# Kernel optimization log

Hardware: AMD Instinct MI355X
Metric: run time of the kernel (lower is better)

The kernel has to match this reference:

```python
import jax, jax.numpy as jnp
import numpy as np

N_BASIS = 8
N_RANK = 4
IN_DIM = 64
B, T = 64, 8192


def _make_projections():
    # Match torch module: np.random.seed(15385); per rank draw E then F, QR, take first n_basis cols.
    np.random.seed(seed=15385)
    Es, Fs = [], []
    for _ in range(N_RANK):
        G = np.random.standard_normal([IN_DIM, IN_DIM])
        Q, _ = np.linalg.qr(G)
        Es.append(Q[:, :N_BASIS])
        G = np.random.standard_normal([IN_DIM, IN_DIM])
        Q, _ = np.linalg.qr(G)
        Fs.append(Q[:, :N_BASIS])
    E = jnp.asarray(np.stack(Es), dtype=jnp.float32)  # [R, C, nb]
    F = jnp.asarray(np.stack(Fs), dtype=jnp.float32)  # [R, C, nb]
    return E, F


def setup_inputs() -> dict:
    key = jax.random.key(0)
    x = jax.random.normal(key, (B, IN_DIM, T), dtype=jnp.float32)
    E, F = _make_projections()
    init_sigma = float(np.sqrt(IN_DIM))
    sigma = jnp.full((N_RANK,), init_sigma, dtype=jnp.float32)
    rho = jnp.full((N_RANK,), init_sigma, dtype=jnp.float32)
    return {"x": x, "sigma": sigma, "rho": rho, "E": E, "F": F}


def reference(x, sigma, rho, E, F):
    # x: [B, C, T]; E,F: [R, C, nb]; sigma,rho: [R]
    in_dim = x.shape[1]
    scale = jnp.sqrt(jnp.float32(in_dim))
    Er = (scale / (1e-05 + jnp.abs(sigma)))[:, None, None] * E  # [R, C, nb]
    Fr = (scale / (1e-05 + jnp.abs(rho)))[:, None, None] * F    # [R, C, nb]
    xe = jnp.einsum('bct,rcn->brtn', x, Er)  # [B, R, T, nb]
    xf = jnp.einsum('bct,rcm->brtm', x, Fr)  # [B, R, T, nb]
    # outer product per (b, t), summed over rank, averaged
    z = jnp.einsum('brtn,brtm->btnm', xe, xf) / jnp.float32(N_RANK)  # [B, T, nb, nb]
    bsz, tlen = x.shape[0], x.shape[2]
    out = z.reshape(bsz, tlen, N_BASIS * N_BASIS).transpose(0, 2, 1)  # [B, nb^2, T]
    # use_normalization=True: signed sqrt + channel max normalization
    out = jnp.sign(out) * (jnp.sqrt(jnp.abs(out) + 0.01) - jnp.float32(np.sqrt(0.01)))
    max_vals = jnp.max(jnp.abs(out), axis=1, keepdims=True)
    out = out / (max_vals + 1e-05)
    return out
```

## Files before the change

### kernel.cpp

```cpp
#include <hip/hip_runtime.h>

#define BB 64
#define CC 64
#define TT 8192
#define NB 8

typedef __attribute__((ext_vector_type(8))) short bf16x8;
typedef __attribute__((ext_vector_type(4))) float f32x4;
typedef __attribute__((ext_vector_type(4))) int i32x4;

union I4B8 { i32x4 i; bf16x8 b; };

__device__ __forceinline__ unsigned short f32_to_bf16_rn(float f) {
    unsigned u = __float_as_uint(f);
    unsigned r = (u + 0x7FFFu + ((u >> 16) & 1u)) >> 16;
    return (unsigned short)r;
}
__device__ __forceinline__ float bf16_to_f32(unsigned short h) {
    return __uint_as_float(((unsigned)h) << 16);
}

__global__ __launch_bounds__(256) void rpg_prep(
    const float* __restrict__ sigma, const float* __restrict__ rho,
    const float* __restrict__ E, const float* __restrict__ F,
    unsigned short* __restrict__ Wf)
{
    const int idx = blockIdx.x * 256 + threadIdx.x;
    if (idx >= 8192) return;
    const int j    = idx & 7;
    const int slot = idx >> 3;
    const int lane = slot & 63;
    const int h    = (slot >> 6) & 1;
    const int ks   = (slot >> 7) & 1;
    const int mt   = (slot >> 8) & 3;
    const int p = mt * 16 + (lane & 15);
    const int c = ks * 32 + (lane >> 4) * 8 + j;
    float val;
    if (p < 32) {
        const int r = p >> 3, n = p & 7;
        const float es = 8.0f / (1e-5f + fabsf(sigma[r]));
        const float fs = 8.0f / (1e-5f + fabsf(rho[r]));
        val = E[r * (CC * NB) + c * NB + n] * (es * fs * 0.25f);
    } else {
        const int r = (p - 32) >> 3, n = p & 7;
        val = F[r * (CC * NB) + c * NB + n];
    }
    const unsigned short hi = f32_to_bf16_rn(val);
    Wf[idx] = (h == 0) ? hi : f32_to_bf16_rn(val - bf16_to_f32(hi));
}

__global__ __launch_bounds__(256, 8) void rpg_main(
    const float* __restrict__ x,
    const unsigned short* __restrict__ Wf,
    float* __restrict__ out)
{
    __shared__ __align__(16) char smem[16384];
    char* xhs = smem;
    char* xls = smem + 8192;

    const int tid  = threadIdx.x;
    const int w    = tid >> 6;
    const int lane = tid & 63;
    const int am   = lane & 15;
    const int ag   = lane >> 4;

    const int b  = blockIdx.x >> 7;
    const int t0 = (blockIdx.x & 127) * 64;

    {
        const float* xcol = x + b * (CC * TT) + t0 + lane;
        unsigned hw[8], lw[8];
        #pragma unroll
        for (int k = 0; k < 8; ++k) {
            const int c = w * 16 + 2 * k;
            const float f0 = xcol[(c    ) * TT];
            const float f1 = xcol[(c + 1) * TT];
            const unsigned u0 = __float_as_uint(f0), u1 = __float_as_uint(f1);
            hw[k] = (u0 >> 16) | (u1 & 0xFFFF0000u);
            const float h0 = __uint_as_float(u0 & 0xFFFF0000u);
            const float h1 = __uint_as_float(u1 & 0xFFFF0000u);
            lw[k] = (__float_as_uint(f0 - h0) >> 16) | (__float_as_uint(f1 - h1) & 0xFFFF0000u);
        }
        const int sw = lane & 7;
        char* hb = xhs + lane * 128;
        char* lb = xls + lane * 128;
        *(i32x4*)(hb + (((2 * w    ) ^ sw) * 16)) = (i32x4){(int)hw[0], (int)hw[1], (int)hw[2], (int)hw[3]};
        *(i32x4*)(hb + (((2 * w + 1) ^ sw) * 16)) = (i32x4){(int)hw[4], (int)hw[5], (int)hw[6], (int)hw[7]};
        *(i32x4*)(lb + (((2 * w    ) ^ sw) * 16)) = (i32x4){(int)lw[0], (int)lw[1], (int)lw[2], (int)lw[3]};
        *(i32x4*)(lb + (((2 * w + 1) ^ sw) * 16)) = (i32x4){(int)lw[4], (int)lw[5], (int)lw[6], (int)lw[7]};
    }
    __syncthreads();

    bf16x8 xh[2], xl[2];
    {
        const int trow = w * 16 + am;
        const int sw   = trow & 7;
        #pragma unroll
        for (int ks = 0; ks < 2; ++ks) {
            const int g  = (ks * 4 + ag) ^ sw;
            const int off = trow * 128 + g * 16;
            xh[ks] = ((const I4B8*)(xhs + off))->b;
            xl[ks] = ((const I4B8*)(xls + off))->b;
        }
    }

    f32x4 acc[4];
    #pragma unroll
    for (int mt = 0; mt < 4; ++mt) {
        acc[mt] = (f32x4){0.0f, 0.0f, 0.0f, 0.0f};
        #pragma unroll
        for (int ks = 0; ks < 2; ++ks) {
            const bf16x8 wh = *(const bf16x8*)(Wf + (((mt * 2 + ks) * 2 + 0) * 64 + lane) * 8);
            const bf16x8 wl = *(const bf16x8*)(Wf + (((mt * 2 + ks) * 2 + 1) * 64 + lane) * 8);
            acc[mt] = __builtin_amdgcn_mfma_f32_16x16x32_bf16(wh, xh[ks], acc[mt], 0, 0, 0);
            acc[mt] = __builtin_amdgcn_mfma_f32_16x16x32_bf16(wh, xl[ks], acc[mt], 0, 0, 0);
            acc[mt] = __builtin_amdgcn_mfma_f32_16x16x32_bf16(wl, xh[ks], acc[mt], 0, 0, 0);
        }
    }

    const bool ra0 = (ag & 2) == 0;
    const bool qlo = (ag & 1) == 0;

    float pA[4], pB[4], pC[4], pD[4];
    #pragma unroll
    for (int i = 0; i < 4; ++i) {
        pA[i] = __shfl_xor(acc[0][i], 32);
        pB[i] = __shfl_xor(acc[1][i], 32);
        pC[i] = __shfl_xor(acc[2][i], 32);
        pD[i] = __shfl_xor(acc[3][i], 32);
    }

    float xe_[4][2];
    #pragma unroll
    for (int e = 0; e < 2; ++e) {
        xe_[0][e] = ra0 ? acc[0][e] : pA[2 + e];
        xe_[1][e] = ra0 ? pA[e]     : acc[0][2 + e];
        xe_[2][e] = ra0 ? acc[1][e] : pB[2 + e];
        xe_[3][e] = ra0 ? pB[e]     : acc[1][2 + e];
    }

    float xfq0[4], xfq1[4], xfq2[4], xfq3[4];
    #pragma unroll
    for (int i = 0; i < 4; ++i) {
        xfq0[i] = ra0 ? acc[2][i] : pC[i];
        xfq1[i] = ra0 ? pC[i]     : acc[2][i];
        xfq2[i] = ra0 ? acc[3][i] : pD[i];
        xfq3[i] = ra0 ? pD[i]     : acc[3][i];
    }
    float xfo0[4], xfo1[4], xfo2[4], xfo3[4];
    #pragma unroll
    for (int i = 0; i < 4; ++i) {
        xfo0[i] = __shfl_xor(xfq0[i], 16);
        xfo1[i] = __shfl_xor(xfq1[i], 16);
        xfo2[i] = __shfl_xor(xfq2[i], 16);
        xfo3[i] = __shfl_xor(xfq3[i], 16);
    }
    float xfL[4][4], xfH[4][4];
    #pragma unroll
    for (int i = 0; i < 4; ++i) {
        xfL[0][i] = qlo ? xfq0[i] : xfo0[i];  xfH[0][i] = qlo ? xfo0[i] : xfq0[i];
        xfL[1][i] = qlo ? xfq1[i] : xfo1[i];  xfH[1][i] = qlo ? xfo1[i] : xfq1[i];
        xfL[2][i] = qlo ? xfq2[i] : xfo2[i];  xfH[2][i] = qlo ? xfo2[i] : xfq2[i];
        xfL[3][i] = qlo ? xfq3[i] : xfo3[i];  xfH[3][i] = qlo ? xfo3[i] : xfq3[i];
    }

    float z[2][8];
    float pm = 0.0f;
    #pragma unroll
    for (int e = 0; e < 2; ++e) {
        #pragma unroll
        for (int m = 0; m < 4; ++m) {
            float a = xe_[0][e] * xfL[0][m];
            a = fmaf(xe_[1][e], xfL[1][m], a);
            a = fmaf(xe_[2][e], xfL[2][m], a);
            a = fmaf(xe_[3][e], xfL[3][m], a);
            float s = __builtin_amdgcn_sqrtf(fabsf(a) + 0.01f) - 0.1f;
            float v = copysignf(s, a);
            z[e][m] = v;
            pm = fmaxf(pm, fabsf(v));
        }
        #pragma unroll
        for (int m = 0; m < 4; ++m) {
            float a = xe_[0][e] * xfH[0][m];
            a = fmaf(xe_[1][e], xfH[1][m], a);
            a = fmaf(xe_[2][e], xfH[2][m], a);
            a = fmaf(xe_[3][e], xfH[3][m], a);
            float s = __builtin_amdgcn_sqrtf(fabsf(a) + 0.01f) - 0.1f;
            float v = copysignf(s, a);
            z[e][4 + m] = v;
            pm = fmaxf(pm, fabsf(v));
        }
    }

    pm = fmaxf(pm, __shfl_xor(pm, 16));
    pm = fmaxf(pm, __shfl_xor(pm, 32));
    const float rinv = __builtin_amdgcn_rcpf(pm + 1e-5f);

    const int nbase = (qlo ? 0 : 4) + (ra0 ? 0 : 2);
    float* ob = out + b * (64 * TT) + t0 + w * 16 + am;
    #pragma unroll
    for (int e = 0; e < 2; ++e)
        #pragma unroll
        for (int m = 0; m < 8; ++m)
            ob[((nbase + e) * NB + m) * TT] = z[e][m] * rinv;
}

extern "C" void kernel_launch(void* const* d_in, const int* in_sizes, int n_in,
                              void* d_out, int out_size, void* d_ws, size_t ws_size,
                              hipStream_t stream) {
    const float* x     = (const float*)d_in[0];
    const float* sigma = (const float*)d_in[1];
    const float* rho   = (const float*)d_in[2];
    const float* E     = (const float*)d_in[3];
    const float* F     = (const float*)d_in[4];
    float* out = (float*)d_out;

    unsigned short* Wf = (unsigned short*)d_ws;

    rpg_prep<<<32, 256, 0, stream>>>(sigma, rho, E, F, Wf);

    dim3 grid(BB * (TT / 64));
    dim3 block(256);
    rpg_main<<<grid, block, 0, stream>>>(x, Wf, out);
}
```

Baseline: 60.67 us.

## Fuse weight prep into persistent kernel with double-buffered x prefetch

Removes the separate weight-preparation kernel: each block now builds the bf16 hi/lo split weights in shared memory itself. The main kernel becomes persistent with a fixed grid of 768 blocks looping over 8192 windows. It prefetches the next window's x into registers while computing the current one, using double-buffered LDS. This saves a launch and global weight loads, at the cost of lower occupancy (48KB LDS, launch bounds 3) and redundant per-block weight setup.

New measurement: 49.84 us. 17.9% less time.

```diff
diff --git a/kernel.cpp b/kernel.cpp
--- a/kernel.cpp
+++ b/kernel.cpp
@@ -1,9 +1,10 @@
 #include <hip/hip_runtime.h>
 
-#define BB 64
 #define CC 64
 #define TT 8192
 #define NB 8
+#define NWIN 8192
+#define GRID 768
 
 typedef __attribute__((ext_vector_type(8))) short bf16x8;
 typedef __attribute__((ext_vector_type(4))) float f32x4;
@@ -20,43 +21,16 @@
     return __uint_as_float(((unsigned)h) << 16);
 }
 
-__global__ __launch_bounds__(256) void rpg_prep(
-    const float* __restrict__ sigma, const float* __restrict__ rho,
-    const float* __restrict__ E, const float* __restrict__ F,
-    unsigned short* __restrict__ Wf)
-{
-    const int idx = blockIdx.x * 256 + threadIdx.x;
-    if (idx >= 8192) return;
-    const int j    = idx & 7;
-    const int slot = idx >> 3;
-    const int lane = slot & 63;
-    const int h    = (slot >> 6) & 1;
-    const int ks   = (slot >> 7) & 1;
-    const int mt   = (slot >> 8) & 3;
-    const int p = mt * 16 + (lane & 15);
-    const int c = ks * 32 + (lane >> 4) * 8 + j;
-    float val;
-    if (p < 32) {
-        const int r = p >> 3, n = p & 7;
-        const float es = 8.0f / (1e-5f + fabsf(sigma[r]));
-        const float fs = 8.0f / (1e-5f + fabsf(rho[r]));
-        val = E[r * (CC * NB) + c * NB + n] * (es * fs * 0.25f);
-    } else {
-        const int r = (p - 32) >> 3, n = p & 7;
-        val = F[r * (CC * NB) + c * NB + n];
-    }
-    const unsigned short hi = f32_to_bf16_rn(val);
-    Wf[idx] = (h == 0) ? hi : f32_to_bf16_rn(val - bf16_to_f32(hi));
-}
-
-__global__ __launch_bounds__(256, 8) void rpg_main(
+__global__ __launch_bounds__(256, 3) void rpg_fused(
     const float* __restrict__ x,
-    const unsigned short* __restrict__ Wf,
+    const float* __restrict__ sigma,
+    const float* __restrict__ rho,
+    const float* __restrict__ E,
+    const float* __restrict__ F,
     float* __restrict__ out)
 {
-    __shared__ __align__(16) char smem[16384];
-    char* xhs = smem;
-    char* xls = smem + 8192;
+    __shared__ __align__(16) char smem[49152];
+    char* wsl = smem;
 
     const int tid  = threadIdx.x;
     const int w    = tid >> 6;
@@ -64,145 +38,207 @@
     const int am   = lane & 15;
     const int ag   = lane >> 4;
 
-    const int b  = blockIdx.x >> 7;
-    const int t0 = (blockIdx.x & 127) * 64;
-
     {
+        const int r = tid >> 6;
+        const int c = tid & 63;
+        const float g = (8.0f / (1e-5f + fabsf(sigma[r]))) *
+                        (8.0f / (1e-5f + fabsf(rho[r]))) * 0.25f;
+        const int wks = c >> 5, wag = (c >> 3) & 3, wj = c & 7;
+        const float4 e0 = *(const float4*)(E + (r * 64 + c) * 8);
+        const float4 e1 = *(const float4*)(E + (r * 64 + c) * 8 + 4);
+        const float4 fv0 = *(const float4*)(F + (r * 64 + c) * 8);
+        const float4 fv1 = *(const float4*)(F + (r * 64 + c) * 8 + 4);
+        const float ev[8] = {e0.x, e0.y, e0.z, e0.w, e1.x, e1.y, e1.z, e1.w};
+        const float fv[8] = {fv0.x, fv0.y, fv0.z, fv0.w, fv1.x, fv1.y, fv1.z, fv1.w};
+        #pragma unroll
+        for (int n = 0; n < 8; ++n) {
+            {
+                const int p = r * 8 + n;
+                const float val = ev[n] * g;
+                const unsigned short hi = f32_to_bf16_rn(val);
+                const unsigned short lo = f32_to_bf16_rn(val - bf16_to_f32(hi));
+                const int mt = p >> 4, pam = p & 15;
+                char* base = wsl + ((((mt * 2 + wks) * 2 + 0) * 64 + wag * 16 + pam) << 4) + wj * 2;
+                *(unsigned short*)base = hi;
+                *(unsigned short*)(base + 1024) = lo;
+            }
+            {
+                const int p = 32 + r * 8 + n;
+                const float val = fv[n];
+                const unsigned short hi = f32_to_bf16_rn(val);
+                const unsigned short lo = f32_to_bf16_rn(val - bf16_to_f32(hi));
+                const int mt = p >> 4, pam = p & 15;
+                char* base = wsl + ((((mt * 2 + wks) * 2 + 0) * 64 + wag * 16 + pam) << 4) + wj * 2;
+                *(unsigned short*)base = hi;
+                *(unsigned short*)(base + 1024) = lo;
+            }
+        }
+    }
+
+    int wid = blockIdx.x;
+    float f[16];
+    {
+        const int b = wid >> 7, t0 = (wid & 127) << 6;
         const float* xcol = x + b * (CC * TT) + t0 + lane;
-        unsigned hw[8], lw[8];
-        #pragma unroll
-        for (int k = 0; k < 8; ++k) {
-            const int c = w * 16 + 2 * k;
-            const float f0 = xcol[(c    ) * TT];
-            const float f1 = xcol[(c + 1) * TT];
-            const unsigned u0 = __float_as_uint(f0), u1 = __float_as_uint(f1);
-            hw[k] = (u0 >> 16) | (u1 & 0xFFFF0000u);
-            const float h0 = __uint_as_float(u0 & 0xFFFF0000u);
-            const float h1 = __uint_as_float(u1 & 0xFFFF0000u);
-            lw[k] = (__float_as_uint(f0 - h0) >> 16) | (__float_as_uint(f1 - h1) & 0xFFFF0000u);
-        }
-        const int sw = lane & 7;
-        char* hb = xhs + lane * 128;
-        char* lb = xls + lane * 128;
-        *(i32x4*)(hb + (((2 * w    ) ^ sw) * 16)) = (i32x4){(int)hw[0], (int)hw[1], (int)hw[2], (int)hw[3]};
-        *(i32x4*)(hb + (((2 * w + 1) ^ sw) * 16)) = (i32x4){(int)hw[4], (int)hw[5], (int)hw[6], (int)hw[7]};
-        *(i32x4*)(lb + (((2 * w    ) ^ sw) * 16)) = (i32x4){(int)lw[0], (int)lw[1], (int)lw[2], (int)lw[3]};
-        *(i32x4*)(lb + (((2 * w + 1) ^ sw) * 16)) = (i32x4){(int)lw[4], (int)lw[5], (int)lw[6], (int)lw[7]};
+        #pragma unroll
+        for (int k = 0; k < 16; ++k) f[k] = xcol[(w * 16 + k) * TT];
     }
-    __syncthreads();
-
-    bf16x8 xh[2], xl[2];
-    {
-        const int trow = w * 16 + am;
-        const int sw   = trow & 7;
-        #pragma unroll
-        for (int ks = 0; ks < 2; ++ks) {
-            const int g  = (ks * 4 + ag) ^ sw;
-            const int off = trow * 128 + g * 16;
-            xh[ks] = ((const I4B8*)(xhs + off))->b;
-            xl[ks] = ((const I4B8*)(xls + off))->b;
-        }
-    }
-
-    f32x4 acc[4];
-    #pragma unroll
-    for (int mt = 0; mt < 4; ++mt) {
-        acc[mt] = (f32x4){0.0f, 0.0f, 0.0f, 0.0f};
-        #pragma unroll
-        for (int ks = 0; ks < 2; ++ks) {
-            const bf16x8 wh = *(const bf16x8*)(Wf + (((mt * 2 + ks) * 2 + 0) * 64 + lane) * 8);
-            const bf16x8 wl = *(const bf16x8*)(Wf + (((mt * 2 + ks) * 2 + 1) * 64 + lane) * 8);
-            acc[mt] = __builtin_amdgcn_mfma_f32_16x16x32_bf16(wh, xh[ks], acc[mt], 0, 0, 0);
-            acc[mt] = __builtin_amdgcn_mfma_f32_16x16x32_bf16(wh, xl[ks], acc[mt], 0, 0, 0);
-            acc[mt] = __builtin_amdgcn_mfma_f32_16x16x32_bf16(wl, xh[ks], acc[mt], 0, 0, 0);
-        }
-    }
-
+
+    int ibuf = 0;
     const bool ra0 = (ag & 2) == 0;
     const bool qlo = (ag & 1) == 0;
 
-    float pA[4], pB[4], pC[4], pD[4];
-    #pragma unroll
-    for (int i = 0; i < 4; ++i) {
-        pA[i] = __shfl_xor(acc[0][i], 32);
-        pB[i] = __shfl_xor(acc[1][i], 32);
-        pC[i] = __shfl_xor(acc[2][i], 32);
-        pD[i] = __shfl_xor(acc[3][i], 32);
+    while (wid < NWIN) {
+        char* xbuf = ibuf ? (smem + 32768) : (smem + 16384);
+
+        {
+            unsigned hw[8], lw[8];
+            #pragma unroll
+            for (int k = 0; k < 8; ++k) {
+                const unsigned u0 = __float_as_uint(f[2 * k]);
+                const unsigned u1 = __float_as_uint(f[2 * k + 1]);
+                hw[k] = (u0 >> 16) | (u1 & 0xFFFF0000u);
+                const float h0 = __uint_as_float(u0 & 0xFFFF0000u);
+                const float h1 = __uint_as_float(u1 & 0xFFFF0000u);
+                lw[k] = (__float_as_uint(f[2 * k] - h0) >> 16) |
+                        (__float_as_uint(f[2 * k + 1] - h1) & 0xFFFF0000u);
+            }
+            const int sw = lane & 7;
+            char* hb = xbuf + lane * 128;
+            char* lb = xbuf + 8192 + lane * 128;
+            *(i32x4*)(hb + (((2 * w    ) ^ sw) * 16)) = (i32x4){(int)hw[0], (int)hw[1], (int)hw[2], (int)hw[3]};
+            *(i32x4*)(hb + (((2 * w + 1) ^ sw) * 16)) = (i32x4){(int)hw[4], (int)hw[5], (int)hw[6], (int)hw[7]};
+            *(i32x4*)(lb + (((2 * w    ) ^ sw) * 16)) = (i32x4){(int)lw[0], (int)lw[1], (int)lw[2], (int)lw[3]};
+            *(i32x4*)(lb + (((2 * w + 1) ^ sw) * 16)) = (i32x4){(int)lw[4], (int)lw[5], (int)lw[6], (int)lw[7]};
+        }
+
+        const int b  = wid >> 7;
+        const int t0 = (wid & 127) << 6;
+        const int next = wid + GRID;
+
+        __syncthreads();
+
+        bf16x8 xh[2], xl[2];
+        {
+            const int trow = w * 16 + am;
+            const int sw   = trow & 7;
+            #pragma unroll
+            for (int ks = 0; ks < 2; ++ks) {
+                const int g2  = (ks * 4 + ag) ^ sw;
+                const int off = trow * 128 + g2 * 16;
+                xh[ks] = ((const I4B8*)(xbuf + off))->b;
+                xl[ks] = ((const I4B8*)(xbuf + 8192 + off))->b;
+            }
+        }
+
+        if (next < NWIN) {
+            const int nbx = next >> 7, nt0 = (next & 127) << 6;
+            const float* xcol = x + nbx * (CC * TT) + nt0 + lane;
+            #pragma unroll
+            for (int k = 0; k < 16; ++k) f[k] = xcol[(w * 16 + k) * TT];
+        }
+
+        f32x4 acc[4];
+        #pragma unroll
+        for (int mt = 0; mt < 4; ++mt) {
+            acc[mt] = (f32x4){0.0f, 0.0f, 0.0f, 0.0f};
+            #pragma unroll
+            for (int ks = 0; ks < 2; ++ks) {
+                const int fb = ((mt * 2 + ks) * 2) * 1024 + lane * 16;
+                const bf16x8 wh = ((const I4B8*)(wsl + fb))->b;
+                const bf16x8 wl = ((const I4B8*)(wsl + fb + 1024))->b;
+                acc[mt] = __builtin_amdgcn_mfma_f32_16x16x32_bf16(wh, xh[ks], acc[mt], 0, 0, 0);
+                acc[mt] = __builtin_amdgcn_mfma_f32_16x16x32_bf16(wh, xl[ks], acc[mt], 0, 0, 0);
+                acc[mt] = __builtin_amdgcn_mfma_f32_16x16x32_bf16(wl, xh[ks], acc[mt], 0, 0, 0);
+            }
+        }
+
+        float pA[4], pB[4], pC[4], pD[4];
+        #pragma unroll
+        for (int i = 0; i < 4; ++i) {
+            pA[i] = __shfl_xor(acc[0][i], 32);
+            pB[i] = __shfl_xor(acc[1][i], 32);
+            pC[i] = __shfl_xor(acc[2][i], 32);
+            pD[i] = __shfl_xor(acc[3][i], 32);
+        }
+
+        float xe_[4][2];
+        #pragma unroll
+        for (int e = 0; e < 2; ++e) {
+            xe_[0][e] = ra0 ? acc[0][e] : pA[2 + e];
+            xe_[1][e] = ra0 ? pA[e]     : acc[0][2 + e];
+            xe_[2][e] = ra0 ? acc[1][e] : pB[2 + e];
+            xe_[3][e] = ra0 ? pB[e]     : acc[1][2 + e];
+        }
+
+        float xfq0[4], xfq1[4], xfq2[4], xfq3[4];
+        #pragma unroll
+        for (int i = 0; i < 4; ++i) {
+            xfq0[i] = ra0 ? acc[2][i] : pC[i];
+            xfq1[i] = ra0 ? pC[i]     : acc[2][i];
+            xfq2[i] = ra0 ? acc[3][i] : pD[i];
+            xfq3[i] = ra0 ? pD[i]     : acc[3][i];
+        }
+        float xfo0[4], xfo1[4], xfo2[4], xfo3[4];
+        #pragma unroll
+        for (int i = 0; i < 4; ++i) {
+            xfo0[i] = __shfl_xor(xfq0[i], 16);
+            xfo1[i] = __shfl_xor(xfq1[i], 16);
+            xfo2[i] = __shfl_xor(xfq2[i], 16);
+            xfo3[i] = __shfl_xor(xfq3[i], 16);
+        }
+        float xfL[4][4], xfH[4][4];
+        #pragma unroll
+        for (int i = 0; i < 4; ++i) {
+            xfL[0][i] = qlo ? xfq0[i] : xfo0[i];  xfH[0][i] = qlo ? xfo0[i] : xfq0[i];
+            xfL[1][i] = qlo ? xfq1[i] : xfo1[i];  xfH[1][i] = qlo ? xfo1[i] : xfq1[i];
+            xfL[2][i] = qlo ? xfq2[i] : xfo2[i];  xfH[2][i] = qlo ? xfo2[i] : xfq2[i];
+            xfL[3][i] = qlo ? xfq3[i] : xfo3[i];  xfH[3][i] = qlo ? xfo3[i] : xfq3[i];
+        }
+
+        float z[2][8];
+        float pm = 0.0f;
+        #pragma unroll
+        for (int e = 0; e < 2; ++e) {
+            #pragma unroll
+            for (int m = 0; m < 4; ++m) {
+                float a = xe_[0][e] * xfL[0][m];
+                a = fmaf(xe_[1][e], xfL[1][m], a);
+                a = fmaf(xe_[2][e], xfL[2][m], a);
+                a = fmaf(xe_[3][e], xfL[3][m], a);
+                float s = __builtin_amdgcn_sqrtf(fabsf(a) + 0.01f) - 0.1f;
+                float v = copysignf(s, a);
+                z[e][m] = v;
+                pm = fmaxf(pm, fabsf(v));
+            }
+            #pragma unroll
+            for (int m = 0; m < 4; ++m) {
+                float a = xe_[0][e] * xfH[0][m];
+                a = fmaf(xe_[1][e], xfH[1][m], a);
+                a = fmaf(xe_[2][e], xfH[2][m], a);
+                a = fmaf(xe_[3][e], xfH[3][m], a);
+                float s = __builtin_amdgcn_sqrtf(fabsf(a) + 0.01f) - 0.1f;
+                float v = copysignf(s, a);
+                z[e][4 + m] = v;
+                pm = fmaxf(pm, fabsf(v));
+            }
+        }
+
+        pm = fmaxf(pm, __shfl_xor(pm, 16));
+        pm = fmaxf(pm, __shfl_xor(pm, 32));
+        const float rinv = __builtin_amdgcn_rcpf(pm + 1e-5f);
+
+        const int nbase = (qlo ? 0 : 4) + (ra0 ? 0 : 2);
+        float* ob = out + b * (64 * TT) + t0 + w * 16 + am;
+        #pragma unroll
+        for (int e = 0; e < 2; ++e)
+            #pragma unroll
+            for (int m = 0; m < 8; ++m)
+                ob[((nbase + e) * NB + m) * TT] = z[e][m] * rinv;
+
+        wid = next;
+        ibuf ^= 1;
     }
-
-    float xe_[4][2];
-    #pragma unroll
-    for (int e = 0; e < 2; ++e) {
-        xe_[0][e] = ra0 ? acc[0][e] : pA[2 + e];
-        xe_[1][e] = ra0 ? pA[e]     : acc[0][2 + e];
-        xe_[2][e] = ra0 ? acc[1][e] : pB[2 + e];
-        xe_[3][e] = ra0 ? pB[e]     : acc[1][2 + e];
-    }
-
-    float xfq0[4], xfq1[4], xfq2[4], xfq3[4];
-    #pragma unroll
-    for (int i = 0; i < 4; ++i) {
-        xfq0[i] = ra0 ? acc[2][i] : pC[i];
-        xfq1[i] = ra0 ? pC[i]     : acc[2][i];
-        xfq2[i] = ra0 ? acc[3][i] : pD[i];
-        xfq3[i] = ra0 ? pD[i]     : acc[3][i];
-    }
-    float xfo0[4], xfo1[4], xfo2[4], xfo3[4];
-    #pragma unroll
-    for (int i = 0; i < 4; ++i) {
-        xfo0[i] = __shfl_xor(xfq0[i], 16);
-        xfo1[i] = __shfl_xor(xfq1[i], 16);
-        xfo2[i] = __shfl_xor(xfq2[i], 16);
-        xfo3[i] = __shfl_xor(xfq3[i], 16);
-    }
-    float xfL[4][4], xfH[4][4];
-    #pragma unroll
-    for (int i = 0; i < 4; ++i) {
-        xfL[0][i] = qlo ? xfq0[i] : xfo0[i];  xfH[0][i] = qlo ? xfo0[i] : xfq0[i];
-        xfL[1][i] = qlo ? xfq1[i] : xfo1[i];  xfH[1][i] = qlo ? xfo1[i] : xfq1[i];
-        xfL[2][i] = qlo ? xfq2[i] : xfo2[i];  xfH[2][i] = qlo ? xfo2[i] : xfq2[i];
-        xfL[3][i] = qlo ? xfq3[i] : xfo3[i];  xfH[3][i] = qlo ? xfo3[i] : xfq3[i];
-    }
-
-    float z[2][8];
-    float pm = 0.0f;
-    #pragma unroll
-    for (int e = 0; e < 2; ++e) {
-        #pragma unroll
-        for (int m = 0; m < 4; ++m) {
-            float a = xe_[0][e] * xfL[0][m];
-            a = fmaf(xe_[1][e], xfL[1][m], a);
-            a = fmaf(xe_[2][e], xfL[2][m], a);
-            a = fmaf(xe_[3][e], xfL[3][m], a);
-            float s = __builtin_amdgcn_sqrtf(fabsf(a) + 0.01f) - 0.1f;
-            float v = copysignf(s, a);
-            z[e][m] = v;
-            pm = fmaxf(pm, fabsf(v));
-        }
-        #pragma unroll
-        for (int m = 0; m < 4; ++m) {
-            float a = xe_[0][e] * xfH[0][m];
-            a = fmaf(xe_[1][e], xfH[1][m], a);
-            a = fmaf(xe_[2][e], xfH[2][m], a);
-            a = fmaf(xe_[3][e], xfH[3][m], a);
-            float s = __builtin_amdgcn_sqrtf(fabsf(a) + 0.01f) - 0.1f;
-            float v = copysignf(s, a);
-            z[e][4 + m] = v;
-            pm = fmaxf(pm, fabsf(v));
-        }
-    }
-
-    pm = fmaxf(pm, __shfl_xor(pm, 16));
-    pm = fmaxf(pm, __shfl_xor(pm, 32));
-    const float rinv = __builtin_amdgcn_rcpf(pm + 1e-5f);
-
-    const int nbase = (qlo ? 0 : 4) + (ra0 ? 0 : 2);
-    float* ob = out + b * (64 * TT) + t0 + w * 16 + am;
-    #pragma unroll
-    for (int e = 0; e < 2; ++e)
-        #pragma unroll
-        for (int m = 0; m < 8; ++m)
-            ob[((nbase + e) * NB + m) * TT] = z[e][m] * rinv;
 }
 
 extern "C" void kernel_launch(void* const* d_in, const int* in_sizes, int n_in,
@@ -215,11 +251,5 @@
     const float* F     = (const float*)d_in[4];
     float* out = (float*)d_out;
 
-    unsigned short* Wf = (unsigned short*)d_ws;
-
-    rpg_prep<<<32, 256, 0, stream>>>(sigma, rho, E, F, Wf);
-
-    dim3 grid(BB * (TT / 64));
-    dim3 block(256);
-    rpg_main<<<grid, block, 0, stream>>>(x, Wf, out);
-}
+    rpg_fused<<<GRID, 256, 0, stream>>>(x, sigma, rho, E, F, out);
+}
```

## Use persistent waves with register-prefetched x tiles and no LDS staging

Applied to the files above, without the earlier changes.

Replaces the one-block-per-64-timesteps grid with a persistent grid of 768 blocks. Each wave loops over 16-timestep tiles and prefetches the next tile's x into registers while it computes the current one. The split weights are loaded into registers once per wave instead of per tile. Each lane now loads x directly in MFMA operand layout, which removes the LDS staging buffer and the barrier. Global loads become 16-wide in t rather than 64-wide, which may reduce coalescing, and register pressure rises.

Result: faster. 59.28 us (-2.3%).

```diff
diff --git a/kernel.cpp b/kernel.cpp
--- a/kernel.cpp
+++ b/kernel.cpp
@@ -1,9 +1,11 @@
 #include <hip/hip_runtime.h>
 
-#define BB 64
 #define CC 64
 #define TT 8192
 #define NB 8
+#define NW16 32768
+#define GRID 768
+#define NWAVES (GRID * 4)
 
 typedef __attribute__((ext_vector_type(8))) short bf16x8;
 typedef __attribute__((ext_vector_type(4))) float f32x4;
@@ -49,160 +51,177 @@
     Wf[idx] = (h == 0) ? hi : f32_to_bf16_rn(val - bf16_to_f32(hi));
 }
 
-__global__ __launch_bounds__(256, 8) void rpg_main(
+__global__ __launch_bounds__(256, 3) void rpg_main(
     const float* __restrict__ x,
     const unsigned short* __restrict__ Wf,
     float* __restrict__ out)
 {
-    __shared__ __align__(16) char smem[16384];
-    char* xhs = smem;
-    char* xls = smem + 8192;
-
     const int tid  = threadIdx.x;
     const int w    = tid >> 6;
     const int lane = tid & 63;
     const int am   = lane & 15;
     const int ag   = lane >> 4;
 
-    const int b  = blockIdx.x >> 7;
-    const int t0 = (blockIdx.x & 127) * 64;
-
-    {
-        const float* xcol = x + b * (CC * TT) + t0 + lane;
-        unsigned hw[8], lw[8];
-        #pragma unroll
-        for (int k = 0; k < 8; ++k) {
-            const int c = w * 16 + 2 * k;
-            const float f0 = xcol[(c    ) * TT];
-            const float f1 = xcol[(c + 1) * TT];
-            const unsigned u0 = __float_as_uint(f0), u1 = __float_as_uint(f1);
-            hw[k] = (u0 >> 16) | (u1 & 0xFFFF0000u);
-            const float h0 = __uint_as_float(u0 & 0xFFFF0000u);
-            const float h1 = __uint_as_float(u1 & 0xFFFF0000u);
-            lw[k] = (__float_as_uint(f0 - h0) >> 16) | (__float_as_uint(f1 - h1) & 0xFFFF0000u);
-        }
-        const int sw = lane & 7;
-        char* hb = xhs + lane * 128;
-        char* lb = xls + lane * 128;
-        *(i32x4*)(hb + (((2 * w    ) ^ sw) * 16)) = (i32x4){(int)hw[0], (int)hw[1], (int)hw[2], (int)hw[3]};
-        *(i32x4*)(hb + (((2 * w + 1) ^ sw) * 16)) = (i32x4){(int)hw[4], (int)hw[5], (int)hw[6], (int)hw[7]};
-        *(i32x4*)(lb + (((2 * w    ) ^ sw) * 16)) = (i32x4){(int)lw[0], (int)lw[1], (int)lw[2], (int)lw[3]};
-        *(i32x4*)(lb + (((2 * w + 1) ^ sw) * 16)) = (i32x4){(int)lw[4], (int)lw[5], (int)lw[6], (int)lw[7]};
-    }
-    __syncthreads();
-
-    bf16x8 xh[2], xl[2];
-    {
-        const int trow = w * 16 + am;
-        const int sw   = trow & 7;
-        #pragma unroll
-        for (int ks = 0; ks < 2; ++ks) {
-            const int g  = (ks * 4 + ag) ^ sw;
-            const int off = trow * 128 + g * 16;
-            xh[ks] = ((const I4B8*)(xhs + off))->b;
-            xl[ks] = ((const I4B8*)(xls + off))->b;
-        }
-    }
-
-    f32x4 acc[4];
+    bf16x8 wfh[8], wfl[8];
     #pragma unroll
-    for (int mt = 0; mt < 4; ++mt) {
-        acc[mt] = (f32x4){0.0f, 0.0f, 0.0f, 0.0f};
-        #pragma unroll
-        for (int ks = 0; ks < 2; ++ks) {
-            const bf16x8 wh = *(const bf16x8*)(Wf + (((mt * 2 + ks) * 2 + 0) * 64 + lane) * 8);
-            const bf16x8 wl = *(const bf16x8*)(Wf + (((mt * 2 + ks) * 2 + 1) * 64 + lane) * 8);
-            acc[mt] = __builtin_amdgcn_mfma_f32_16x16x32_bf16(wh, xh[ks], acc[mt], 0, 0, 0);
-            acc[mt] = __builtin_amdgcn_mfma_f32_16x16x32_bf16(wh, xl[ks], acc[mt], 0, 0, 0);
-            acc[mt] = __builtin_amdgcn_mfma_f32_16x16x32_bf16(wl, xh[ks], acc[mt], 0, 0, 0);
-        }
+    for (int s = 0; s < 8; ++s) {
+        wfh[s] = *(const bf16x8*)(Wf + ((s * 2 + 0) * 64 + lane) * 8);
+        wfl[s] = *(const bf16x8*)(Wf + ((s * 2 + 1) * 64 + lane) * 8);
     }
 
     const bool ra0 = (ag & 2) == 0;
     const bool qlo = (ag & 1) == 0;
 
-    float pA[4], pB[4], pC[4], pD[4];
-    #pragma unroll
-    for (int i = 0; i < 4; ++i) {
-        pA[i] = __shfl_xor(acc[0][i], 32);
-        pB[i] = __shfl_xor(acc[1][i], 32);
-        pC[i] = __shfl_xor(acc[2][i], 32);
-        pD[i] = __shfl_xor(acc[3][i], 32);
-    }
-
-    float xe_[4][2];
-    #pragma unroll
-    for (int e = 0; e < 2; ++e) {
-        xe_[0][e] = ra0 ? acc[0][e] : pA[2 + e];
-        xe_[1][e] = ra0 ? pA[e]     : acc[0][2 + e];
-        xe_[2][e] = ra0 ? acc[1][e] : pB[2 + e];
-        xe_[3][e] = ra0 ? pB[e]     : acc[1][2 + e];
-    }
-
-    float xfq0[4], xfq1[4], xfq2[4], xfq3[4];
-    #pragma unroll
-    for (int i = 0; i < 4; ++i) {
-        xfq0[i] = ra0 ? acc[2][i] : pC[i];
-        xfq1[i] = ra0 ? pC[i]     : acc[2][i];
-        xfq2[i] = ra0 ? acc[3][i] : pD[i];
-        xfq3[i] = ra0 ? pD[i]     : acc[3][i];
-    }
-    float xfo0[4], xfo1[4], xfo2[4], xfo3[4];
-    #pragma unroll
-    for (int i = 0; i < 4; ++i) {
-        xfo0[i] = __shfl_xor(xfq0[i], 16);
-        xfo1[i] = __shfl_xor(xfq1[i], 16);
-        xfo2[i] = __shfl_xor(xfq2[i], 16);
-        xfo3[i] = __shfl_xor(xfq3[i], 16);
-    }
-    float xfL[4][4], xfH[4][4];
-    #pragma unroll
-    for (int i = 0; i < 4; ++i) {
-        xfL[0][i] = qlo ? xfq0[i] : xfo0[i];  xfH[0][i] = qlo ? xfo0[i] : xfq0[i];
-        xfL[1][i] = qlo ? xfq1[i] : xfo1[i];  xfH[1][i] = qlo ? xfo1[i] : xfq1[i];
-        xfL[2][i] = qlo ? xfq2[i] : xfo2[i];  xfH[2][i] = qlo ? xfo2[i] : xfq2[i];
-        xfL[3][i] = qlo ? xfq3[i] : xfo3[i];  xfH[3][i] = qlo ? xfo3[i] : xfq3[i];
-    }
-
-    float z[2][8];
-    float pm = 0.0f;
-    #pragma unroll
-    for (int e = 0; e < 2; ++e) {
-        #pragma unroll
-        for (int m = 0; m < 4; ++m) {
-            float a = xe_[0][e] * xfL[0][m];
-            a = fmaf(xe_[1][e], xfL[1][m], a);
-            a = fmaf(xe_[2][e], xfL[2][m], a);
-            a = fmaf(xe_[3][e], xfL[3][m], a);
-            float s = __builtin_amdgcn_sqrtf(fabsf(a) + 0.01f) - 0.1f;
-            float v = copysignf(s, a);
-            z[e][m] = v;
-            pm = fmaxf(pm, fabsf(v));
-        }
-        #pragma unroll
-        for (int m = 0; m < 4; ++m) {
-            float a = xe_[0][e] * xfH[0][m];
-            a = fmaf(xe_[1][e], xfH[1][m], a);
-            a = fmaf(xe_[2][e], xfH[2][m], a);
-            a = fmaf(xe_[3][e], xfH[3][m], a);
-            float s = __builtin_amdgcn_sqrtf(fabsf(a) + 0.01f) - 0.1f;
-            float v = copysignf(s, a);
-            z[e][4 + m] = v;
-            pm = fmaxf(pm, fabsf(v));
-        }
-    }
-
-    pm = fmaxf(pm, __shfl_xor(pm, 16));
-    pm = fmaxf(pm, __shfl_xor(pm, 32));
-    const float rinv = __builtin_amdgcn_rcpf(pm + 1e-5f);
-
-    const int nbase = (qlo ? 0 : 4) + (ra0 ? 0 : 2);
-    float* ob = out + b * (64 * TT) + t0 + w * 16 + am;
-    #pragma unroll
-    for (int e = 0; e < 2; ++e)
-        #pragma unroll
-        for (int m = 0; m < 8; ++m)
-            ob[((nbase + e) * NB + m) * TT] = z[e][m] * rinv;
+    int wid = blockIdx.x * 4 + w;
+
+    float f[16];
+    {
+        const int b = wid >> 9, t0 = (wid & 511) << 4;
+        const float* xp = x + b * (CC * TT) + t0 + am;
+        #pragma unroll
+        for (int k = 0; k < 16; ++k) {
+            const int c = ((k >> 3) * 32) + ag * 8 + (k & 7);
+            f[k] = xp[c * TT];
+        }
+    }
+
+    #pragma unroll 1
+    while (wid < NW16) {
+        bf16x8 xh[2], xl[2];
+        #pragma unroll
+        for (int ks = 0; ks < 2; ++ks) {
+            unsigned hw[4], lw[4];
+            #pragma unroll
+            for (int k = 0; k < 4; ++k) {
+                const float f0 = f[ks * 8 + 2 * k];
+                const float f1 = f[ks * 8 + 2 * k + 1];
+                const unsigned u0 = __float_as_uint(f0), u1 = __float_as_uint(f1);
+                hw[k] = (u0 >> 16) | (u1 & 0xFFFF0000u);
+                const float h0 = __uint_as_float(u0 & 0xFFFF0000u);
+                const float h1 = __uint_as_float(u1 & 0xFFFF0000u);
+                lw[k] = (__float_as_uint(f0 - h0) >> 16) |
+                        (__float_as_uint(f1 - h1) & 0xFFFF0000u);
+            }
+            I4B8 H, L;
+            H.i = (i32x4){(int)hw[0], (int)hw[1], (int)hw[2], (int)hw[3]};
+            L.i = (i32x4){(int)lw[0], (int)lw[1], (int)lw[2], (int)lw[3]};
+            xh[ks] = H.b;
+            xl[ks] = L.b;
+        }
+
+        const int b  = wid >> 9;
+        const int t0 = (wid & 511) << 4;
+        const int nxt = wid + NWAVES;
+
+        if (nxt < NW16) {
+            const int nb = nxt >> 9, nt0 = (nxt & 511) << 4;
+            const float* xp = x + nb * (CC * TT) + nt0 + am;
+            #pragma unroll
+            for (int k = 0; k < 16; ++k) {
+                const int c = ((k >> 3) * 32) + ag * 8 + (k & 7);
+                f[k] = xp[c * TT];
+            }
+        }
+
+        f32x4 acc[4];
+        #pragma unroll
+        for (int mt = 0; mt < 4; ++mt) {
+            acc[mt] = (f32x4){0.0f, 0.0f, 0.0f, 0.0f};
+            #pragma unroll
+            for (int ks = 0; ks < 2; ++ks) {
+                const bf16x8 wh = wfh[mt * 2 + ks];
+                const bf16x8 wl = wfl[mt * 2 + ks];
+                acc[mt] = __builtin_amdgcn_mfma_f32_16x16x32_bf16(wh, xh[ks], acc[mt], 0, 0, 0);
+                acc[mt] = __builtin_amdgcn_mfma_f32_16x16x32_bf16(wh, xl[ks], acc[mt], 0, 0, 0);
+                acc[mt] = __builtin_amdgcn_mfma_f32_16x16x32_bf16(wl, xh[ks], acc[mt], 0, 0, 0);
+            }
+        }
+
+        float pA[4], pB[4], pC[4], pD[4];
+        #pragma unroll
+        for (int i = 0; i < 4; ++i) {
+            pA[i] = __shfl_xor(acc[0][i], 32);
+            pB[i] = __shfl_xor(acc[1][i], 32);
+            pC[i] = __shfl_xor(acc[2][i], 32);
+            pD[i] = __shfl_xor(acc[3][i], 32);
+        }
+
+        float xe_[4][2];
+        #pragma unroll
+        for (int e = 0; e < 2; ++e) {
+            xe_[0][e] = ra0 ? acc[0][e] : pA[2 + e];
+            xe_[1][e] = ra0 ? pA[e]     : acc[0][2 + e];
+            xe_[2][e] = ra0 ? acc[1][e] : pB[2 + e];
+            xe_[3][e] = ra0 ? pB[e]     : acc[1][2 + e];
+        }
+
+        float xfq0[4], xfq1[4], xfq2[4], xfq3[4];
+        #pragma unroll
+        for (int i = 0; i < 4; ++i) {
+            xfq0[i] = ra0 ? acc[2][i] : pC[i];
+            xfq1[i] = ra0 ? pC[i]     : acc[2][i];
+            xfq2[i] = ra0 ? acc[3][i] : pD[i];
+            xfq3[i] = ra0 ? pD[i]     : acc[3][i];
+        }
+        float xfo0[4], xfo1[4], xfo2[4], xfo3[4];
+        #pragma unroll
+        for (int i = 0; i < 4; ++i) {
+            xfo0[i] = __shfl_xor(xfq0[i], 16);
+            xfo1[i] = __shfl_xor(xfq1[i], 16);
+            xfo2[i] = __shfl_xor(xfq2[i], 16);
+            xfo3[i] = __shfl_xor(xfq3[i], 16);
+        }
+        float xfL[4][4], xfH[4][4];
+        #pragma unroll
+        for (int i = 0; i < 4; ++i) {
+            xfL[0][i] = qlo ? xfq0[i] : xfo0[i];  xfH[0][i] = qlo ? xfo0[i] : xfq0[i];
+            xfL[1][i] = qlo ? xfq1[i] : xfo1[i];  xfH[1][i] = qlo ? xfo1[i] : xfq1[i];
+            xfL[2][i] = qlo ? xfq2[i] : xfo2[i];  xfH[2][i] = qlo ? xfo2[i] : xfq2[i];
+            xfL[3][i] = qlo ? xfq3[i] : xfo3[i];  xfH[3][i] = qlo ? xfo3[i] : xfq3[i];
+        }
+
+        float z[2][8];
+        float pm = 0.0f;
+        #pragma unroll
+        for (int e = 0; e < 2; ++e) {
+            #pragma unroll
+            for (int m = 0; m < 4; ++m) {
+                float a = xe_[0][e] * xfL[0][m];
+                a = fmaf(xe_[1][e], xfL[1][m], a);
+                a = fmaf(xe_[2][e], xfL[2][m], a);
+                a = fmaf(xe_[3][e], xfL[3][m], a);
+                float s = __builtin_amdgcn_sqrtf(fabsf(a) + 0.01f) - 0.1f;
+                float v = copysignf(s, a);
+                z[e][m] = v;
+                pm = fmaxf(pm, fabsf(v));
+            }
+            #pragma unroll
+            for (int m = 0; m < 4; ++m) {
+                float a = xe_[0][e] * xfH[0][m];
+                a = fmaf(xe_[1][e], xfH[1][m], a);
+                a = fmaf(xe_[2][e], xfH[2][m], a);
+                a = fmaf(xe_[3][e], xfH[3][m], a);
+                float s = __builtin_amdgcn_sqrtf(fabsf(a) + 0.01f) - 0.1f;
+                float v = copysignf(s, a);
+                z[e][4 + m] = v;
+                pm = fmaxf(pm, fabsf(v));
+            }
+        }
+
+        pm = fmaxf(pm, __shfl_xor(pm, 16));
+        pm = fmaxf(pm, __shfl_xor(pm, 32));
+        const float rinv = __builtin_amdgcn_rcpf(pm + 1e-5f);
+
+        const int nbase = (qlo ? 0 : 4) + (ra0 ? 0 : 2);
+        float* ob = out + b * (64 * TT) + t0 + am;
+        #pragma unroll
+        for (int e = 0; e < 2; ++e)
+            #pragma unroll
+            for (int m = 0; m < 8; ++m)
+                ob[((nbase + e) * NB + m) * TT] = z[e][m] * rinv;
+
+        wid = nxt;
+    }
 }
 
 extern "C" void kernel_launch(void* const* d_in, const int* in_sizes, int n_in,
@@ -219,7 +238,5 @@
 
     rpg_prep<<<32, 256, 0, stream>>>(sigma, rho, E, F, Wf);
 
-    dim3 grid(BB * (TT / 64));
-    dim3 block(256);
-    rpg_main<<<grid, block, 0, stream>>>(x, Wf, out);
-}
+    rpg_main<<<GRID, 256, 0, stream>>>(x, Wf, out);
+}
```
